# Kernel optimization log

Hardware: AMD Instinct MI355X
Metric: run time of the kernel (lower is better)

## Reference

```python
import jax, jax.numpy as jnp
import numpy as np

B, T, D_IN, H = 64, 512, 768, 512
FC1, FC2 = 512, 256
LN_EPS = 1e-3  # Keras LayerNormalization default epsilon


def setup_inputs() -> dict:
    key = jax.random.key(0)
    ks = jax.random.split(key, 20)
    sc = 0.05
    n = lambda i, shape: jax.random.normal(ks[i], shape, jnp.float32) * sc
    return {
        "x": jax.random.normal(ks[0], (B, T, D_IN), jnp.float32),
        "mask": jnp.ones((B, T), dtype=bool),
        # forward-direction LSTM (Keras gate order i, f, c, o along 4H axis)
        "W_f": n(1, (D_IN, 4 * H)), "U_f": n(2, (H, 4 * H)), "b_f": jnp.zeros((4 * H,), jnp.float32),
        # backward-direction LSTM
        "W_b": n(3, (D_IN, 4 * H)), "U_b": n(4, (H, 4 * H)), "b_b": jnp.zeros((4 * H,), jnp.float32),
        # layernorm over last dim (2H)
        "ln_gamma": jnp.ones((2 * H,), jnp.float32), "ln_beta": jnp.zeros((2 * H,), jnp.float32),
        # attention scorer Dense(1)
        "attn_w": n(5, (2 * H, 1)), "attn_b": jnp.zeros((1,), jnp.float32),
        # FC stack: 2H -> FC1 (relu) -> FC2 (tanh)
        "fc1_w": n(6, (2 * H, FC1)), "fc1_b": jnp.zeros((FC1,), jnp.float32),
        "fc2_w": n(7, (FC1, FC2)), "fc2_b": jnp.zeros((FC2,), jnp.float32),
    }


def _lstm_scan(x, mask, W, U, b, reverse):
    """Keras-style masked LSTM. x: [B,T,D], mask: [B,T] -> [B,T,H]."""
    xs = jnp.swapaxes(x, 0, 1)            # [T,B,D]
    ms = jnp.swapaxes(mask, 0, 1)         # [T,B]
    if reverse:
        xs, ms = xs[::-1], ms[::-1]
    gx = xs @ W + b                       # precompute input gates [T,B,4H]

    def step(carry, inp):
        h, c = carry
        g, m = inp
        z = g + h @ U                     # [B,4H]
        i, f, cc, o = jnp.split(z, 4, axis=-1)
        c_new = jax.nn.sigmoid(f) * c + jax.nn.sigmoid(i) * jnp.tanh(cc)
        h_new = jax.nn.sigmoid(o) * jnp.tanh(c_new)
        m = m[:, None]
        h2 = jnp.where(m, h_new, h)       # masked step: carry state, repeat output
        c2 = jnp.where(m, c_new, c)
        return (h2, c2), h2

    h0 = jnp.zeros((x.shape[0], U.shape[0]), x.dtype)
    (_, _), hs = jax.lax.scan(step, (h0, h0), (gx, ms))
    if reverse:
        hs = hs[::-1]
    return jnp.swapaxes(hs, 0, 1)         # [B,T,H]


def reference(x, mask, W_f, U_f, b_f, W_b, U_b, b_b, ln_gamma, ln_beta,
              attn_w, attn_b, fc1_w, fc1_b, fc2_w, fc2_b):
    hf = _lstm_scan(x, mask, W_f, U_f, b_f, reverse=False)
    hb = _lstm_scan(x, mask, W_b, U_b, b_b, reverse=True)
    hiddens = jnp.concatenate([hf, hb], axis=-1)          # [B,T,2H]
    mu = jnp.mean(hiddens, axis=-1, keepdims=True)
    var = jnp.mean(jnp.square(hiddens - mu), axis=-1, keepdims=True)
    hn = (hiddens - mu) * jax.lax.rsqrt(var + LN_EPS) * ln_gamma + ln_beta
    scores = jnp.squeeze(hn @ attn_w, axis=-1) + attn_b[0]  # [B,T]
    weights = jax.nn.softmax(scores, axis=-1)
    context = jnp.einsum('bt,btd->bd', weights, hn)        # [B,2H]
    context = jax.nn.relu(context @ fc1_w + fc1_b)
    context = jnp.tanh(context @ fc2_w + fc2_b)
    return (hn, context)
```

## Files before the change

### kernel.cpp

```cpp
#include <hip/hip_runtime.h>
#include <cstdint>
#include <cstddef>

#define B_   64
#define T_   512
#define DIN_ 768
#define H_   512

typedef _Float16 half8_t __attribute__((ext_vector_type(8)));
typedef _Float16 half4_t __attribute__((ext_vector_type(4)));
typedef float    float4_t __attribute__((ext_vector_type(4)));
typedef int      int4_v   __attribute__((ext_vector_type(4)));
typedef int      int2_v   __attribute__((ext_vector_type(2)));

static constexpr size_t OFF_XT   = 0;
static constexpr size_t SZ_XT    = (size_t)T_*B_*DIN_*2;
static constexpr size_t OFF_WP   = OFF_XT + SZ_XT;
static constexpr size_t SZ_WP    = (size_t)2*128*24*64*8*2;
static constexpr size_t OFF_UP   = OFF_WP + SZ_WP;
static constexpr size_t SZ_UP    = (size_t)2*128*16*64*8*2;
static constexpr size_t OFF_GX   = OFF_UP + SZ_UP;
static constexpr size_t SZ_GX    = (size_t)2*T_*B_*4*H_*2;
static constexpr size_t OFF_HB   = OFF_GX + SZ_GX;
static constexpr size_t SZ_HB    = (size_t)8*2*8192*2;
static constexpr size_t OFF_FLAG = OFF_HB + SZ_HB;
static constexpr size_t SZ_FLAG  = 4096;
static constexpr size_t OFF_SC   = OFF_FLAG + SZ_FLAG;
static constexpr size_t SZ_SC    = (size_t)B_*T_*4;
static constexpr size_t OFF_WT   = OFF_SC + SZ_SC;
static constexpr size_t SZ_WT    = SZ_SC;
static constexpr size_t OFF_CTX  = OFF_WT + SZ_WT;
static constexpr size_t SZ_CTX   = (size_t)B_*1024*4;
static constexpr size_t WS_NEED  = OFF_CTX + SZ_CTX;

__device__ __forceinline__ float fsig(float x) {
  return __builtin_amdgcn_rcpf(1.f + __expf(-x));
}
__device__ __forceinline__ float ftanh_(float x) {
  return 1.f - 2.f * __builtin_amdgcn_rcpf(__expf(2.f * x) + 1.f);
}

__device__ __forceinline__ void mall_load_b128(half8_t& dst, const _Float16* p) {
  asm volatile("global_load_dwordx4 %0, %1, off sc0 sc1"
               : "=v"(dst) : "v"(p) : "memory");
}
__device__ __forceinline__ void mall_load_b64(half4_t& dst, const _Float16* p) {
  asm volatile("global_load_dwordx2 %0, %1, off sc0 sc1"
               : "=v"(dst) : "v"(p) : "memory");
}
__device__ __forceinline__ void mall_store_b128(_Float16* p, int4_v v) {
  asm volatile("global_store_dwordx4 %0, %1, off sc0 sc1"
               :: "v"(p), "v"(v) : "memory");
}
__device__ __forceinline__ void mall_store_b64(_Float16* p, int2_v v) {
  asm volatile("global_store_dwordx2 %0, %1, off sc0 sc1"
               :: "v"(p), "v"(v) : "memory");
}

__device__ __forceinline__ void wg_barrier_lds() {
  asm volatile("s_waitcnt lgkmcnt(0)\n\ts_barrier" ::: "memory");
}

__device__ __forceinline__ unsigned pack_tag(float a, float b, unsigned tagd) {
  unsigned lo = (unsigned)__builtin_bit_cast(unsigned short, (_Float16)a);
  unsigned hi = (unsigned)__builtin_bit_cast(unsigned short, (_Float16)b);
  return (((hi << 16) | lo) & 0xFFFEFFFEu) | tagd;
}

__global__ __launch_bounds__(256) void transpose_x(const float* __restrict__ x,
                                                   _Float16* __restrict__ xt)
{
  const int t  = blockIdx.x >> 3;
  const int bc = blockIdx.x & 7;
  #pragma unroll
  for (int r = 0; r < 8; ++r) {
    const int b = bc * 8 + r;
    const float* src = x + ((size_t)b * T_ + t) * DIN_;
    _Float16*    dst = xt + ((size_t)t * B_ + b) * DIN_;
    for (int i = threadIdx.x; i < DIN_; i += 256) dst[i] = (_Float16)src[i];
  }
}

__global__ __launch_bounds__(256) void pack_w(const float* __restrict__ src,
                                              _Float16* __restrict__ dst, int Kt)
{
  const int wid  = blockIdx.x * 4 + (threadIdx.x >> 6);
  const int lane = threadIdx.x & 63;
  const int nt = wid / Kt, kt = wid % Kt;
  const int g4 = nt >> 5, s = (nt >> 2) & 7, w2 = nt & 3;
  const int n  = g4 * 512 + s * 64 + w2 * 16 + (lane & 15);
  const int kb = kt * 32 + (lane >> 4) * 8;
  half8_t v;
  #pragma unroll
  for (int e = 0; e < 8; ++e) v[e] = (_Float16)src[(size_t)(kb + e) * 2048 + n];
  *(half8_t*)(dst + ((size_t)wid * 64 + lane) * 8) = v;
}

__device__ void gemm_body(int fgi, int tid, const _Float16* __restrict__ xt,
    const _Float16* __restrict__ wp, const float* __restrict__ bias_f,
    const float* __restrict__ bias_b, _Float16* __restrict__ gx, char* smem)
{
  const int np   = fgi & 7;
  const int rest = fgi >> 3;
  const int d    = rest & 1;
  const int mt_l = rest >> 1;
  const int mt   = d ? (255 - mt_l) : mt_l;
  const int half = tid >> 8;
  const int tl   = tid & 255;
  const int ntb  = np * 2 + half;
  const int lane = tl & 63;
  const int wave = tl >> 6, wrow = wave >> 1, wcol = wave & 1;
  _Float16* As = (_Float16*)smem + (size_t)half * 8192;
  _Float16* Bs = (_Float16*)smem + 16384 + (size_t)half * 8192;

  float4_t acc[4][4];
  #pragma unroll
  for (int i = 0; i < 4; ++i)
    #pragma unroll
    for (int jj = 0; jj < 4; ++jj) acc[i][jj] = float4_t{0.f, 0.f, 0.f, 0.f};
  const int m0 = mt * 128;
  const size_t wbase = ((size_t)d * 128 + ntb * 8) * 24;

  for (int kb = 0; kb < 12; ++kb) {
    #pragma unroll
    for (int i2 = 0; i2 < 4; ++i2) {
      const int slot = i2 * 256 + tl;
      const int l = slot & 63, rt = (slot >> 6) & 7, kk = slot >> 9;
      const int wslot = slot >> 6;
      const _Float16* ga = xt + (size_t)(m0 + rt * 16 + (l & 15)) * DIN_
                              + kb * 64 + kk * 32 + (l >> 4) * 8;
      const _Float16* gb = wp + ((wbase + (size_t)rt * 24 + kb * 2 + kk) * 64 + l) * 8;
      __builtin_amdgcn_global_load_lds(
          (const __attribute__((address_space(1))) void*)ga,
          (__attribute__((address_space(3))) void*)(As + (size_t)wslot * 64 * 8), 16, 0, 0);
      __builtin_amdgcn_global_load_lds(
          (const __attribute__((address_space(1))) void*)gb,
          (__attribute__((address_space(3))) void*)(Bs + (size_t)wslot * 64 * 8), 16, 0, 0);
    }
    __syncthreads();
    #pragma unroll
    for (int kk = 0; kk < 2; ++kk) {
      half8_t af[4], bf[4];
      #pragma unroll
      for (int i = 0; i < 4; ++i)
        af[i] = *(const half8_t*)(As + ((size_t)kk * 512 + (wrow * 4 + i) * 64 + lane) * 8);
      #pragma unroll
      for (int jj = 0; jj < 4; ++jj)
        bf[jj] = *(const half8_t*)(Bs + ((size_t)kk * 512 + (wcol * 4 + jj) * 64 + lane) * 8);
      #pragma unroll
      for (int i = 0; i < 4; ++i)
        #pragma unroll
        for (int jj = 0; jj < 4; ++jj)
          acc[i][jj] = __builtin_amdgcn_mfma_f32_16x16x32_f16(af[i], bf[jj], acc[i][jj], 0, 0, 0);
    }
    __syncthreads();
  }
  const float* bias = d ? bias_b : bias_f;
  const int t = mt * 2 + wrow;
  #pragma unroll
  for (int jj = 0; jj < 4; ++jj) {
    const int ntg = ntb * 8 + wcol * 4 + jj;
    const int g4 = ntg >> 5, s = (ntg >> 2) & 7, w2 = ntg & 3;
    const float bv = bias[g4 * 512 + s * 64 + w2 * 16 + (lane & 15)];
    #pragma unroll
    for (int i = 0; i < 4; ++i) {
      unsigned lo = pack_tag(acc[i][jj][0] + bv, acc[i][jj][1] + bv, 0x00010001u);
      unsigned hi = pack_tag(acc[i][jj][2] + bv, acc[i][jj][3] + bv, 0x00010001u);
      int2_v dv; dv[0] = (int)lo; dv[1] = (int)hi;
      const size_t off = (((((size_t)d * T_ + t) * 4 + i) * 8 + s) * 4 + w2) * 4 + g4;
      mall_store_b64(gx + off * 256 + lane * 4, dv);
    }
  }
}

template<int E0>
__device__ __forceinline__ void lstm_tail(const float4_t* acc, const half4_t* gxv,
    float& c0, float& c1, float* hn_slot, int lane, int jloc)
{
  #pragma unroll
  for (int ee = 0; ee < 2; ++ee) {
    const int e2 = E0 + ee;
    const float zi = acc[0][e2] + (float)gxv[0][e2];
    const float zf = acc[1][e2] + (float)gxv[1][e2];
    const float zc = acc[2][e2] + (float)gxv[2][e2];
    const float zo = acc[3][e2] + (float)gxv[3][e2];
    float& c = ee ? c1 : c0;
    const float cn = fsig(zf) * c + fsig(zi) * ftanh_(zc);
    c = cn;
    const float h = fsig(zo) * ftanh_(cn);
    const int r = ((lane >> 4) << 2) + e2;
    hn_slot[r * 68 + jloc] = h;
  }
}

__device__ void lstm_body(int blk, int tid, const _Float16* __restrict__ gx,
    const _Float16* __restrict__ upack, _Float16* __restrict__ hbuf,
    float* __restrict__ out, char* smem)
{
  const int g8 = blk & 7, s = blk >> 3;
  const int d = g8 >> 2, g = g8 & 3;
  const int lane = tid & 63, wave = tid >> 6;
  const int w2 = wave & 3, kh = wave >> 2;
  float4_t (*partials)[4][64] = (float4_t(*)[4][64])smem;
  float* hn_lds = (float*)(smem + 32768);
  _Float16* frag_lds = (_Float16*)(smem + 32768 + 34816);

  half8_t uf[4][8];
  #pragma unroll
  for (int g4 = 0; g4 < 4; ++g4) {
    const int nt = g4 * 32 + s * 4 + w2;
    #pragma unroll
    for (int k2 = 0; k2 < 8; ++k2) {
      const int kt = kh * 8 + k2;
      uf[g4][k2] = *(const half8_t*)(upack + ((size_t)((d * 128 + nt) * 16 + kt) * 64 + lane) * 8);
    }
  }
  float c0 = 0.f, c1 = 0.f;
  const int jloc = w2 * 16 + (lane & 15);
  const bool own_wave = (wave == s);
  const int ktA = 2 * wave, ktB = ktA + 1;
  _Float16* hb = hbuf + (size_t)g8 * 2 * 8192;

  half4_t gxC[4];
  {
    const int tp0 = d ? (T_ - 1) : 0;
    #pragma unroll
    for (int g4 = 0; g4 < 4; ++g4) {
      const size_t o0 = (((((size_t)d * T_ + tp0) * 4 + g) * 8 + s) * 4 + w2) * 4 + g4;
      mall_load_b64(gxC[g4], gx + o0 * 256 + (size_t)lane * 4);
    }
  }

  for (int t = 0; t < T_; ++t) {
    const _Float16* hsrc = hb + (t & 1) * 8192;
    const int tagpat = ((t >> 1) & 1) ? 0x00010001 : 0;

    half8_t fA, fB;
    if (own_wave) {
      if (t == 0) {
        #pragma unroll
        for (int e = 0; e < 8; ++e) { fA[e] = (_Float16)0.f; fB[e] = (_Float16)0.f; }
      } else {
        const int base = (((t - 1) & 7) * 16 + (lane & 15)) * 68 + ((lane >> 4) * 8);
        const float4_t u0 = *(const float4_t*)&hn_lds[base];
        const float4_t u1 = *(const float4_t*)&hn_lds[base + 4];
        const float4_t u2 = *(const float4_t*)&hn_lds[base + 32];
        const float4_t u3 = *(const float4_t*)&hn_lds[base + 36];
        #pragma unroll
        for (int e = 0; e < 4; ++e) {
          fA[e] = (_Float16)u0[e]; fA[4 + e] = (_Float16)u1[e];
          fB[e] = (_Float16)u2[e]; fB[4 + e] = (_Float16)u3[e];
        }
      }
    } else {
      const _Float16* pA = hsrc + ((size_t)ktA * 64 + lane) * 8;
      const _Float16* pB = hsrc + ((size_t)ktB * 64 + lane) * 8;
      int guard = 0;
      while (true) {
        mall_load_b128(fA, pA);
        mall_load_b128(fB, pB);
        asm volatile("s_waitcnt vmcnt(0)" ::: "memory");
        __builtin_amdgcn_sched_barrier(0);
        const int4_v wA = __builtin_bit_cast(int4_v, fA);
        const int4_v wB = __builtin_bit_cast(int4_v, fB);
        int ok = 1;
        #pragma unroll
        for (int dw = 0; dw < 4; ++dw) {
          ok &= ((wA[dw] & 0x00010001) == tagpat);
          ok &= ((wB[dw] & 0x00010001) == tagpat);
        }
        if (__all(ok)) break;
        if (++guard > (1 << 16)) break;
      }
    }

    asm volatile("s_waitcnt vmcnt(0)" ::: "memory");
    __builtin_amdgcn_sched_barrier(0);
    {
      int guard = 0;
      while (true) {
        int gok = 1;
        #pragma unroll
        for (int g4 = 0; g4 < 4; ++g4) {
          const int2_v w = __builtin_bit_cast(int2_v, gxC[g4]);
          gok &= ((w[0] & 0x00010001) == 0x00010001);
          gok &= ((w[1] & 0x00010001) == 0x00010001);
        }
        if (__all(gok)) break;
        if (++guard > (1 << 16)) break;
        const int tpc = d ? (T_ - 1 - t) : t;
        #pragma unroll
        for (int g4 = 0; g4 < 4; ++g4) {
          const size_t goff = (((((size_t)d * T_ + tpc) * 4 + g) * 8 + s) * 4 + w2) * 4 + g4;
          mall_load_b64(gxC[g4], gx + goff * 256 + (size_t)lane * 4);
        }
        asm volatile("s_waitcnt vmcnt(0)" ::: "memory");
        __builtin_amdgcn_sched_barrier(0);
      }
    }
    half4_t gxv[4];
    #pragma unroll
    for (int g4 = 0; g4 < 4; ++g4) gxv[g4] = gxC[g4];
    if (t + 1 < T_) {
      const int tpn = d ? (T_ - 2 - t) : (t + 1);
      #pragma unroll
      for (int g4 = 0; g4 < 4; ++g4) {
        const size_t goff = (((((size_t)d * T_ + tpn) * 4 + g) * 8 + s) * 4 + w2) * 4 + g4;
        mall_load_b64(gxC[g4], gx + goff * 256 + (size_t)lane * 4);
      }
    }
    if (t >= 7) {
      const int sl  = (t + 1) & 7;
      const int ts  = t - 7;
      const int tpp = d ? (T_ - 1 - ts) : ts;
      #pragma unroll
      for (int rr = 0; rr < 2; ++rr) {
        const int r = wave * 2 + rr;
        const float hv = hn_lds[(sl * 16 + r) * 68 + lane];
        out[((size_t)(g * 16 + r) * T_ + tpp) * 1024 + (size_t)d * H_ + s * 64 + lane] = hv;
      }
    }

    *(half8_t*)(frag_lds + ((size_t)ktA * 64 + lane) * 8) = fA;
    *(half8_t*)(frag_lds + ((size_t)ktB * 64 + lane) * 8) = fB;
    wg_barrier_lds();

    half8_t a[8];
    #pragma unroll
    for (int k2 = 0; k2 < 8; ++k2)
      a[k2] = *(const half8_t*)(frag_lds + ((size_t)(kh * 8 + k2) * 64 + lane) * 8);

    float4_t acc[4] = { {0,0,0,0}, {0,0,0,0}, {0,0,0,0}, {0,0,0,0} };
    #pragma unroll
    for (int k2 = 0; k2 < 8; ++k2)
      #pragma unroll
      for (int g4 = 0; g4 < 4; ++g4)
        acc[g4] = __builtin_amdgcn_mfma_f32_16x16x32_f16(a[k2], uf[g4][k2], acc[g4], 0, 0, 0);

    #pragma unroll
    for (int g4 = 0; g4 < 4; ++g4) partials[wave][g4][lane] = acc[g4];
    wg_barrier_lds();
    #pragma unroll
    for (int g4 = 0; g4 < 4; ++g4) {
      const float4_t p = partials[wave ^ 4][g4][lane];
      acc[g4][0] += p[0]; acc[g4][1] += p[1]; acc[g4][2] += p[2]; acc[g4][3] += p[3];
    }

    float* hn_slot = &hn_lds[(t & 7) * 16 * 68];
    if (kh == 0) lstm_tail<0>(acc, gxv, c0, c1, hn_slot, lane, jloc);
    else         lstm_tail<2>(acc, gxv, c0, c1, hn_slot, lane, jloc);

    wg_barrier_lds();

    if (t + 1 < T_ && lane < 16) {
      const unsigned tagd = (unsigned)(((t + 1) >> 1) & 1) * 0x00010001u;
      const float* src = &hn_lds[((t & 7) * 16 + lane) * 68 + kh * 32 + w2 * 8];
      const float4_t u0 = *(const float4_t*)src;
      const float4_t u1 = *(const float4_t*)(src + 4);
      int4_v dv;
      dv[0] = (int)pack_tag(u0[0], u0[1], tagd);
      dv[1] = (int)pack_tag(u0[2], u0[3], tagd);
      dv[2] = (int)pack_tag(u1[0], u1[1], tagd);
      dv[3] = (int)pack_tag(u1[2], u1[3], tagd);
      mall_store_b128(hb + ((t + 1) & 1) * 8192 + s * 1024 + (wave * 16 + lane) * 8, dv);
    }
  }

  if (wave >= 1) {
    const int ts  = T_ - 8 + wave;
    const int tpp = d ? (T_ - 1 - ts) : ts;
    #pragma unroll
    for (int r = 0; r < 16; ++r) {
      const float hv = hn_lds[(wave * 16 + r) * 68 + lane];
      out[((size_t)(g * 16 + r) * T_ + tpp) * 1024 + (size_t)d * H_ + s * 64 + lane] = hv;
    }
  }
}

__global__ __launch_bounds__(512, 1) void fused_gx_lstm(
    const _Float16* __restrict__ xt, const _Float16* __restrict__ wp,
    const float* __restrict__ b_f, const float* __restrict__ b_b,
    _Float16* __restrict__ gx, const _Float16* __restrict__ upack,
    _Float16* __restrict__ hbuf, float* __restrict__ out)
{
  __shared__ __align__(16) char smem[83968];
  if (blockIdx.x < 64) lstm_body(blockIdx.x, threadIdx.x, gx, upack, hbuf, out, smem);
  else                 gemm_body(blockIdx.x - 64, threadIdx.x, xt, wp, b_f, b_b, gx, smem);
}

__global__ __launch_bounds__(256) void ln_score(float* __restrict__ hn,
    const float* __restrict__ gamma, const float* __restrict__ beta,
    const float* __restrict__ aw, const float* __restrict__ ab,
    float* __restrict__ scores)
{
  const int row = blockIdx.x;
  const int tid = threadIdx.x;
  float* rp = hn + (size_t)row * 1024;
  float v[4]; float sum = 0.f, sum2 = 0.f;
  #pragma unroll
  for (int i = 0; i < 4; ++i) { v[i] = rp[tid + i * 256]; sum += v[i]; sum2 += v[i] * v[i]; }
  #pragma unroll
  for (int m = 32; m >= 1; m >>= 1) { sum += __shfl_xor(sum, m, 64); sum2 += __shfl_xor(sum2, m, 64); }
  __shared__ float rs[4], rs2[4], rs3[4];
  const int wv = tid >> 6;
  if ((tid & 63) == 0) { rs[wv] = sum; rs2[wv] = sum2; }
  __syncthreads();
  sum  = rs[0] + rs[1] + rs[2] + rs[3];
  sum2 = rs2[0] + rs2[1] + rs2[2] + rs2[3];
  const float mu   = sum * (1.f / 1024.f);
  const float var  = sum2 * (1.f / 1024.f) - mu * mu;
  const float rstd = rsqrtf(var + 1e-3f);
  float sacc = 0.f;
  #pragma unroll
  for (int i = 0; i < 4; ++i) {
    const int c = tid + i * 256;
    const float hv = (v[i] - mu) * rstd * gamma[c] + beta[c];
    rp[c] = hv;
    sacc += hv * aw[c];
  }
  #pragma unroll
  for (int m = 32; m >= 1; m >>= 1) sacc += __shfl_xor(sacc, m, 64);
  if ((tid & 63) == 0) rs3[wv] = sacc;
  __syncthreads();
  if (tid == 0) scores[row] = rs3[0] + rs3[1] + rs3[2] + rs3[3] + ab[0];
}

__global__ __launch_bounds__(256) void softmax_k(const float* __restrict__ sc,
                                                 float* __restrict__ wt)
{
  const int b = blockIdx.x, tid = threadIdx.x;
  const float s0 = sc[b * 512 + tid], s1 = sc[b * 512 + 256 + tid];
  float mx = fmaxf(s0, s1);
  #pragma unroll
  for (int m = 32; m >= 1; m >>= 1) mx = fmaxf(mx, __shfl_xor(mx, m, 64));
  __shared__ float r1[4], r2[4];
  const int wv = tid >> 6;
  if ((tid & 63) == 0) r1[wv] = mx;
  __syncthreads();
  mx = fmaxf(fmaxf(r1[0], r1[1]), fmaxf(r1[2], r1[3]));
  const float e0 = __expf(s0 - mx), e1 = __expf(s1 - mx);
  float ss = e0 + e1;
  #pragma unroll
  for (int m = 32; m >= 1; m >>= 1) ss += __shfl_xor(ss, m, 64);
  if ((tid & 63) == 0) r2[wv] = ss;
  __syncthreads();
  ss = r2[0] + r2[1] + r2[2] + r2[3];
  const float inv = 1.f / ss;
  wt[b * 512 + tid] = e0 * inv;
  wt[b * 512 + 256 + tid] = e1 * inv;
}

__global__ __launch_bounds__(256) void ctx_k(const float* __restrict__ hn,
    const float* __restrict__ wt, float* __restrict__ ctx)
{
  const int b  = blockIdx.y;
  const int jj = blockIdx.x * 256 + threadIdx.x;
  const float* base = hn + (size_t)b * 512 * 1024 + jj;
  const float* wb   = wt + b * 512;
  float acc = 0.f;
  #pragma unroll 4
  for (int t = 0; t < 512; ++t) acc += wb[t] * base[(size_t)t * 1024];
  ctx[b * 1024 + jj] = acc;
}

__global__ __launch_bounds__(512) void fc_k(const float* __restrict__ ctx,
    const float* __restrict__ w1, const float* __restrict__ b1,
    const float* __restrict__ w2, const float* __restrict__ b2,
    float* __restrict__ outc)
{
  const int b = blockIdx.x, tid = threadIdx.x;
  __shared__ float cs[1024];
  __shared__ float h1[512];
  cs[tid]       = ctx[b * 1024 + tid];
  cs[tid + 512] = ctx[b * 1024 + 512 + tid];
  __syncthreads();
  float a = b1[tid];
  #pragma unroll 8
  for (int k = 0; k < 1024; ++k) a += cs[k] * w1[(size_t)k * 512 + tid];
  h1[tid] = fmaxf(a, 0.f);
  __syncthreads();
  if (tid < 256) {
    float a2 = b2[tid];
    #pragma unroll 8
    for (int k = 0; k < 512; ++k) a2 += h1[k] * w2[(size_t)k * 256 + tid];
    outc[b * 256 + tid] = tanhf(a2);
  }
}

extern "C" void kernel_launch(void* const* d_in, const int* in_sizes, int n_in,
                              void* d_out, int out_size, void* d_ws, size_t ws_size,
                              hipStream_t stream)
{
  (void)in_sizes; (void)n_in;
  const float* x   = (const float*)d_in[0];
  const float* W_f = (const float*)d_in[2];
  const float* U_f = (const float*)d_in[3];
  const float* b_f = (const float*)d_in[4];
  const float* W_b = (const float*)d_in[5];
  const float* U_b = (const float*)d_in[6];
  const float* b_b = (const float*)d_in[7];
  const float* gam = (const float*)d_in[8];
  const float* bet = (const float*)d_in[9];
  const float* aw  = (const float*)d_in[10];
  const float* ab  = (const float*)d_in[11];
  const float* w1  = (const float*)d_in[12];
  const float* b1  = (const float*)d_in[13];
  const float* w2  = (const float*)d_in[14];
  const float* b2  = (const float*)d_in[15];

  char*  ws  = (char*)d_ws;
  float* out = (float*)d_out;

  if (ws_size < WS_NEED) {
    hipMemsetAsync(d_out, 0x7F, (size_t)out_size * 4, stream);
    return;
  }

  _Float16* xt  = (_Float16*)(ws + OFF_XT);
  _Float16* wp  = (_Float16*)(ws + OFF_WP);
  _Float16* up  = (_Float16*)(ws + OFF_UP);
  _Float16* gx  = (_Float16*)(ws + OFF_GX);
  _Float16* hb  = (_Float16*)(ws + OFF_HB);
  float* scores = (float*)(ws + OFF_SC);
  float* wts    = (float*)(ws + OFF_WT);
  float* ctx    = (float*)(ws + OFF_CTX);

  hipMemsetAsync(ws + OFF_GX, 0, SZ_GX, stream);
  for (int g8 = 0; g8 < 8; ++g8) {
    hipMemsetAsync(ws + OFF_HB + (size_t)g8 * 32768,         0x00, 16384, stream);
    hipMemsetAsync(ws + OFF_HB + (size_t)g8 * 32768 + 16384, 0x01, 16384, stream);
  }

  transpose_x<<<4096, 256, 0, stream>>>(x, xt);
  pack_w<<<768, 256, 0, stream>>>(W_f, wp, 24);
  pack_w<<<768, 256, 0, stream>>>(W_b, wp + (size_t)128 * 24 * 64 * 8, 24);
  pack_w<<<512, 256, 0, stream>>>(U_f, up, 16);
  pack_w<<<512, 256, 0, stream>>>(U_b, up + (size_t)128 * 16 * 64 * 8, 16);
  fused_gx_lstm<<<64 + 4096, 512, 0, stream>>>(xt, wp, b_f, b_b, gx, up, hb, out);
  ln_score<<<32768, 256, 0, stream>>>(out, gam, bet, aw, ab, scores);
  softmax_k<<<64, 256, 0, stream>>>(scores, wts);
  ctx_k<<<dim3(4, 64), 256, 0, stream>>>(out, wts, ctx);
  fc_k<<<64, 512, 0, stream>>>(ctx, w1, b1, w2, b2, out + (size_t)B_ * T_ * 1024);
}
```

Before: 1.795 ms.

## Throttle gx GEMM blocks behind LSTM progress and share A tile across halves

Adds a global progress counter that LSTM block 0 publishes every four timesteps. Late GEMM blocks spin (with sleeps) until the recurrence has advanced far enough, so they do not steal bandwidth or CUs from the latency-critical LSTM blocks too early. The GEMM A tile (x rows) is now loaded once per block by half 0 and shared, instead of each half loading its own copy, which halves x traffic. The spin-wait adds polling overhead, relies on OFF_FLAG/SZ_FLAG being defined elsewhere, and could serialize GEMM work if the throttle is too strict.

```diff
diff --git a/kernel.cpp b/kernel.cpp
--- a/kernel.cpp
+++ b/kernel.cpp
@@ -98,7 +98,8 @@
 
 __device__ void gemm_body(int fgi, int tid, const _Float16* __restrict__ xt,
     const _Float16* __restrict__ wp, const float* __restrict__ bias_f,
-    const float* __restrict__ bias_b, _Float16* __restrict__ gx, char* smem)
+    const float* __restrict__ bias_b, _Float16* __restrict__ gx,
+    const int* __restrict__ prog, char* smem)
 {
   const int np   = fgi & 7;
   const int rest = fgi >> 3;
@@ -110,8 +111,26 @@
   const int ntb  = np * 2 + half;
   const int lane = tl & 63;
   const int wave = tl >> 6, wrow = wave >> 1, wcol = wave & 1;
-  _Float16* As = (_Float16*)smem + (size_t)half * 8192;
-  _Float16* Bs = (_Float16*)smem + 16384 + (size_t)half * 8192;
+  _Float16* As = (_Float16*)smem;
+  _Float16* Bs = (_Float16*)(smem + 16384) + (size_t)half * 8192;
+
+  const int need = 2 * mt_l - 96;
+  if (need > 0) {
+    if (tid == 0) {
+      int guard = 0;
+      while (guard++ < 4096) {
+        int pt;
+        asm volatile("global_load_dword %0, %1, off sc0 sc1"
+                     : "=v"(pt) : "v"(prog) : "memory");
+        asm volatile("s_waitcnt vmcnt(0)" ::: "memory");
+        __builtin_amdgcn_sched_barrier(0);
+        if (pt >= need) break;
+        #pragma unroll
+        for (int ii = 0; ii < 4; ++ii) __builtin_amdgcn_s_sleep(64);
+      }
+    }
+    __syncthreads();
+  }
 
   float4_t acc[4][4];
   #pragma unroll
@@ -127,15 +146,17 @@
       const int slot = i2 * 256 + tl;
       const int l = slot & 63, rt = (slot >> 6) & 7, kk = slot >> 9;
       const int wslot = slot >> 6;
-      const _Float16* ga = xt + (size_t)(m0 + rt * 16 + (l & 15)) * DIN_
-                              + kb * 64 + kk * 32 + (l >> 4) * 8;
       const _Float16* gb = wp + ((wbase + (size_t)rt * 24 + kb * 2 + kk) * 64 + l) * 8;
-      __builtin_amdgcn_global_load_lds(
-          (const __attribute__((address_space(1))) void*)ga,
-          (__attribute__((address_space(3))) void*)(As + (size_t)wslot * 64 * 8), 16, 0, 0);
       __builtin_amdgcn_global_load_lds(
           (const __attribute__((address_space(1))) void*)gb,
           (__attribute__((address_space(3))) void*)(Bs + (size_t)wslot * 64 * 8), 16, 0, 0);
+      if (half == 0) {
+        const _Float16* ga = xt + (size_t)(m0 + rt * 16 + (l & 15)) * DIN_
+                                + kb * 64 + kk * 32 + (l >> 4) * 8;
+        __builtin_amdgcn_global_load_lds(
+            (const __attribute__((address_space(1))) void*)ga,
+            (__attribute__((address_space(3))) void*)(As + (size_t)wslot * 64 * 8), 16, 0, 0);
+      }
     }
     __syncthreads();
     #pragma unroll
@@ -195,7 +216,7 @@
 
 __device__ void lstm_body(int blk, int tid, const _Float16* __restrict__ gx,
     const _Float16* __restrict__ upack, _Float16* __restrict__ hbuf,
-    float* __restrict__ out, char* smem)
+    int* __restrict__ prog, float* __restrict__ out, char* smem)
 {
   const int g8 = blk & 7, s = blk >> 3;
   const int d = g8 >> 2, g = g8 & 3;
@@ -234,6 +255,11 @@
   for (int t = 0; t < T_; ++t) {
     const _Float16* hsrc = hb + (t & 1) * 8192;
     const int tagpat = ((t >> 1) & 1) ? 0x00010001 : 0;
+
+    if (blk == 0 && tid == 0 && (t & 3) == 0) {
+      asm volatile("global_store_dword %0, %1, off sc0 sc1"
+                   :: "v"(prog), "v"(t) : "memory");
+    }
 
     half8_t fA, fB;
     if (own_wave) {
@@ -381,11 +407,11 @@
     const _Float16* __restrict__ xt, const _Float16* __restrict__ wp,
     const float* __restrict__ b_f, const float* __restrict__ b_b,
     _Float16* __restrict__ gx, const _Float16* __restrict__ upack,
-    _Float16* __restrict__ hbuf, float* __restrict__ out)
+    _Float16* __restrict__ hbuf, int* __restrict__ prog, float* __restrict__ out)
 {
   __shared__ __align__(16) char smem[83968];
-  if (blockIdx.x < 64) lstm_body(blockIdx.x, threadIdx.x, gx, upack, hbuf, out, smem);
-  else                 gemm_body(blockIdx.x - 64, threadIdx.x, xt, wp, b_f, b_b, gx, smem);
+  if (blockIdx.x < 64) lstm_body(blockIdx.x, threadIdx.x, gx, upack, hbuf, prog, out, smem);
+  else                 gemm_body(blockIdx.x - 64, threadIdx.x, xt, wp, b_f, b_b, gx, prog, smem);
 }
 
 __global__ __launch_bounds__(256) void ln_score(float* __restrict__ hn,
@@ -521,11 +547,13 @@
   _Float16* up  = (_Float16*)(ws + OFF_UP);
   _Float16* gx  = (_Float16*)(ws + OFF_GX);
   _Float16* hb  = (_Float16*)(ws + OFF_HB);
+  int*   prog   = (int*)(ws + OFF_FLAG);
   float* scores = (float*)(ws + OFF_SC);
   float* wts    = (float*)(ws + OFF_WT);
   float* ctx    = (float*)(ws + OFF_CTX);
 
   hipMemsetAsync(ws + OFF_GX, 0, SZ_GX, stream);
+  hipMemsetAsync(ws + OFF_FLAG, 0, SZ_FLAG, stream);
   for (int g8 = 0; g8 < 8; ++g8) {
     hipMemsetAsync(ws + OFF_HB + (size_t)g8 * 32768,         0x00, 16384, stream);
     hipMemsetAsync(ws + OFF_HB + (size_t)g8 * 32768 + 16384, 0x01, 16384, stream);
@@ -536,7 +564,7 @@
   pack_w<<<768, 256, 0, stream>>>(W_b, wp + (size_t)128 * 24 * 64 * 8, 24);
   pack_w<<<512, 256, 0, stream>>>(U_f, up, 16);
   pack_w<<<512, 256, 0, stream>>>(U_b, up + (size_t)128 * 16 * 64 * 8, 16);
-  fused_gx_lstm<<<64 + 4096, 512, 0, stream>>>(xt, wp, b_f, b_b, gx, up, hb, out);
+  fused_gx_lstm<<<64 + 4096, 512, 0, stream>>>(xt, wp, b_f, b_b, gx, up, hb, prog, out);
   ln_score<<<32768, 256, 0, stream>>>(out, gam, bet, aw, ab, scores);
   softmax_k<<<64, 256, 0, stream>>>(scores, wts);
   ctx_k<<<dim3(4, 64), 256, 0, stream>>>(out, wts, ctx);
```

Result: faster. 1.729 ms (-3.7%).
